# Kernel tuning notes

Measured on AMD Instinct MI355X. Metric: run time of the kernel, lower is better.

The kernel has to match this reference:

```python
import math
import jax, jax.numpy as jnp
import numpy as np

S = 2048
D_MOD = 1024
D_K = 64
D_V = 64
H = 16
MASKED = True


def setup_inputs() -> dict:
    key = jax.random.key(0)
    ks = jax.random.split(key, 11)
    sc_in = 1.0 / math.sqrt(D_MOD)
    sc_o = 1.0 / math.sqrt(H * D_V)
    return {
        "Q_input": jax.random.normal(ks[0], (S, D_MOD), jnp.float32),
        "K_input": jax.random.normal(ks[1], (S, D_MOD), jnp.float32),
        "V_input": jax.random.normal(ks[2], (S, D_MOD), jnp.float32),
        # stacked per-head Linear params (torch Linear: y = x @ W.T + b)
        "WQw": jax.random.uniform(ks[3], (H, D_K, D_MOD), jnp.float32, -sc_in, sc_in),
        "WQb": jax.random.uniform(ks[4], (H, D_K), jnp.float32, -sc_in, sc_in),
        "WKw": jax.random.uniform(ks[5], (H, D_K, D_MOD), jnp.float32, -sc_in, sc_in),
        "WKb": jax.random.uniform(ks[6], (H, D_K), jnp.float32, -sc_in, sc_in),
        "WVw": jax.random.uniform(ks[7], (H, D_V, D_MOD), jnp.float32, -sc_in, sc_in),
        "WVb": jax.random.uniform(ks[8], (H, D_V), jnp.float32, -sc_in, sc_in),
        "WOw": jax.random.uniform(ks[9], (D_MOD, H * D_V), jnp.float32, -sc_o, sc_o),
        "WOb": jax.random.uniform(ks[10], (D_MOD,), jnp.float32, -sc_o, sc_o),
    }


def reference(Q_input, K_input, V_input, WQw, WQb, WKw, WKb, WVw, WVb, WOw, WOb):
    # per-head projections, batched over heads: [H, S, d]
    q = jnp.einsum("sd,hkd->hsk", Q_input, WQw) + WQb[:, None, :]
    k = jnp.einsum("sd,hkd->hsk", K_input, WKw) + WKb[:, None, :]
    v = jnp.einsum("sd,hvd->hsv", V_input, WVw) + WVb[:, None, :]
    # raw scores [H, S, T]
    qk = jnp.einsum("hsk,htk->hst", q, k)
    if MASKED:
        qk = jnp.tril(qk)  # torch.tril: zero (not -inf) upper triangle
    # torch log_softmax(dim=0) on each [S, T] matrix -> axis 1 of [H, S, T]
    scores = jax.nn.log_softmax(qk / math.sqrt(D_K), axis=1)
    attn = jnp.einsum("hst,htv->hsv", scores, v)  # [H, S, d_v]
    # torch.cat(head_attns, dim=1) -> [S, H*d_v], head-major feature order
    Z = jnp.transpose(attn, (1, 0, 2)).reshape(S, H * D_V)
    return Z @ WOw.T + WOb
```

## Files before the change

kernel.cpp:

```cpp
#include <hip/hip_runtime.h>
#include <math.h>
#include <stdint.h>

#define S 2048
#define DMOD 1024
#define H 16

typedef unsigned short ushort_t;
typedef short bf16x8 __attribute__((ext_vector_type(8)));
typedef float f32x4 __attribute__((ext_vector_type(4)));

#define SW(r) ((((r) & 7)) ^ ((((r) >> 3) & 3) << 1))

__device__ __forceinline__ ushort_t f2b(float f) {
    union { float f; unsigned u; } x; x.f = f;
    return (ushort_t)((x.u + 0x7FFFu + ((x.u >> 16) & 1u)) >> 16);
}
__device__ __forceinline__ float b2f(ushort_t b) {
    union { unsigned u; float f; } x; x.u = ((unsigned)b) << 16;
    return x.f;
}
__device__ __forceinline__ void gld16(const ushort_t* g, ushort_t* l) {
    __builtin_amdgcn_global_load_lds(
        (const __attribute__((address_space(1))) unsigned int*)g,
        (__attribute__((address_space(3))) unsigned int*)l, 16, 0, 0);
}

__global__ __launch_bounds__(256) void init_all(
    float* __restrict__ attn_raw, float* __restrict__ out,
    float* __restrict__ sumexp, float* __restrict__ corr)
{
    const int b = blockIdx.x;
    const float4 z4 = {0.f, 0.f, 0.f, 0.f};
    if (b < 2048) {
        *(float4*)(attn_raw + ((size_t)b * 256 + threadIdx.x) * 4) = z4;
    } else if (b < 4096) {
        *(float4*)(out + ((size_t)(b - 2048) * 256 + threadIdx.x) * 4) = z4;
    } else if (b < 4128) {
        int e = ((b - 4096) * 256 + threadIdx.x) * 4;
        float4 v = {(float)(e & 2047), (float)((e + 1) & 2047),
                    (float)((e + 2) & 2047), (float)((e + 3) & 2047)};
        *(float4*)(sumexp + e) = v;
    } else {
        *(float4*)(corr + threadIdx.x * 4) = z4;
    }
}

__global__ __launch_bounds__(256) void convert_all(
    const float* q, const float* k, const float* v,
    const float* wq, const float* wk, const float* wv, const float* wo,
    ushort_t* qo, ushort_t* ko, ushort_t* vo,
    ushort_t* wqo, ushort_t* wko, ushort_t* wvo, ushort_t* woo)
{
    const int seg = blockIdx.y;
    const float* src; ushort_t* dst; size_t off = 0;
    const size_t M1 = (size_t)1 << 20;
    if (seg < 2)       { src = q;  dst = qo;  off = (size_t)seg * M1; }
    else if (seg < 4)  { src = k;  dst = ko;  off = (size_t)(seg - 2) * M1; }
    else if (seg < 6)  { src = v;  dst = vo;  off = (size_t)(seg - 4) * M1; }
    else if (seg == 6) { src = wq; dst = wqo; }
    else if (seg == 7) { src = wk; dst = wko; }
    else if (seg == 8) { src = wv; dst = wvo; }
    else               { src = wo; dst = woo; }
    size_t i = off + ((size_t)blockIdx.x * 256 + threadIdx.x) * 4;
    float4 f = *(const float4*)(src + i);
    union { uint2 u2; ushort_t us[4]; } o;
    o.us[0] = f2b(f.x); o.us[1] = f2b(f.y); o.us[2] = f2b(f.z); o.us[3] = f2b(f.w);
    *(uint2*)(dst + i) = o.u2;
}

__global__ __launch_bounds__(256) void gemm_qkv(
    const ushort_t* __restrict__ A0, const ushort_t* __restrict__ A1,
    const ushort_t* __restrict__ A2, const ushort_t* __restrict__ Wqkv,
    const float* __restrict__ b0, const float* __restrict__ b1,
    const float* __restrict__ b2,
    ushort_t* __restrict__ qbb, ushort_t* __restrict__ kbb,
    ushort_t* __restrict__ vt)
{
    __shared__ ushort_t As[128 * 64];
    __shared__ ushort_t Bs[64 * 64];
    const int tid = threadIdx.x;
    const int lane = tid & 63, wid = tid >> 6;
    const int quad = lane >> 4, l15 = lane & 15;
    const int wr = wid >> 1, wc = wid & 1;
    const int m0 = blockIdx.y * 128;
    const int n0 = blockIdx.x * 64;
    const int seg = n0 >> 10;
    const int nloc = n0 & 1023;
    const ushort_t* A = seg == 0 ? A0 : (seg == 1 ? A1 : A2);
    const float* bias = seg == 0 ? b0 : (seg == 1 ? b1 : b2);

    const f32x4 fz = {0.f, 0.f, 0.f, 0.f};
    f32x4 acc[4][2];
#pragma unroll
    for (int i = 0; i < 4; ++i) { acc[i][0] = fz; acc[i][1] = fz; }

    for (int k0 = 0; k0 < DMOD; k0 += 64) {
        __syncthreads();
#pragma unroll
        for (int i = 0; i < 4; ++i) {
            int c = i * 256 + tid, row = c >> 3, kcl = c & 7;
            gld16(A + (size_t)(m0 + row) * DMOD + k0 + (kcl ^ SW(row)) * 8, &As[c * 8]);
        }
#pragma unroll
        for (int i = 0; i < 2; ++i) {
            int c = i * 256 + tid, row = c >> 3, kcl = c & 7;
            gld16(Wqkv + (size_t)(n0 + row) * DMOD + k0 + (kcl ^ SW(row)) * 8, &Bs[c * 8]);
        }
        __syncthreads();
#pragma unroll
        for (int kc = 0; kc < 2; ++kc) {
            bf16x8 af[4], bfr[2];
#pragma unroll
            for (int mi = 0; mi < 4; ++mi) {
                int row = wr * 64 + mi * 16 + l15;
                af[mi] = *(const bf16x8*)&As[row * 64 + ((kc * 4 + quad) ^ SW(row)) * 8];
            }
#pragma unroll
            for (int ni = 0; ni < 2; ++ni) {
                int row = wc * 32 + ni * 16 + l15;
                bfr[ni] = *(const bf16x8*)&Bs[row * 64 + ((kc * 4 + quad) ^ SW(row)) * 8];
            }
#pragma unroll
            for (int mi = 0; mi < 4; ++mi)
#pragma unroll
                for (int ni = 0; ni < 2; ++ni)
                    acc[mi][ni] = __builtin_amdgcn_mfma_f32_16x16x32_bf16(
                        af[mi], bfr[ni], acc[mi][ni], 0, 0, 0);
        }
    }

    if (seg < 2) {
        ushort_t* C = seg == 0 ? qbb : kbb;
#pragma unroll
        for (int mi = 0; mi < 4; ++mi)
#pragma unroll
            for (int ni = 0; ni < 2; ++ni) {
                int gn = nloc + wc * 32 + ni * 16 + l15;
                float bv = bias[gn];
#pragma unroll
                for (int r = 0; r < 4; ++r) {
                    int gm = m0 + wr * 64 + mi * 16 + quad * 4 + r;
                    C[(size_t)gm * DMOD + gn] = f2b(acc[mi][ni][r] + bv);
                }
            }
    } else {
#pragma unroll
        for (int mi = 0; mi < 4; ++mi)
#pragma unroll
            for (int ni = 0; ni < 2; ++ni) {
                int gn = nloc + wc * 32 + ni * 16 + l15;
                float bv = bias[gn];
                int gmb = m0 + wr * 64 + mi * 16 + quad * 4;
                union { uint2 u2; ushort_t us[4]; } o;
#pragma unroll
                for (int r = 0; r < 4; ++r) o.us[r] = f2b(acc[mi][ni][r] + bv);
                *(uint2*)&vt[(size_t)gn * S + gmb] = o.u2;
            }
    }
}

__global__ __launch_bounds__(512, 4) void attn_mfma(
    const ushort_t* __restrict__ qb, const ushort_t* __restrict__ kb,
    const ushort_t* __restrict__ vt, float* __restrict__ attn_raw,
    float* __restrict__ sumexp)
{
    __shared__ ushort_t Qs[128 * 64];
    __shared__ ushort_t Ks[2][4096];
    __shared__ ushort_t Vs[2][4096];
    __shared__ ushort_t Ps[128 * 64];
    __shared__ float    sacc[1024];

    const int h = blockIdx.y;
    const int bx = blockIdx.x;
    const int si = 15 - (bx >> 1);
    const int z = bx & 1;
    const int half = si + 1;
    const int tbeg = z ? half : 0;
    const int tend = z ? 2 * si + 2 : half;
    const int s0 = si * 128;

    const int tid = threadIdx.x;
    const int lane = tid & 63, w = tid >> 6;
    const int quad = lane >> 4, l15 = lane & 15;
    const int sband = s0 + w * 16;

    const ushort_t* qh = qb + h * 64;
    const ushort_t* kh = kb + h * 64;
    const ushort_t* vh = vt + (size_t)(h * 64) * S;

#pragma unroll
    for (int i = 0; i < 2; ++i) {
        int c = i * 512 + tid, row = c >> 3, kcl = c & 7;
        gld16(qh + (size_t)(s0 + row) * DMOD + (kcl ^ SW(row)) * 8, &Qs[c * 8]);
    }
    {
        int t0 = tbeg * 64;
        int row = tid >> 3, kcl = tid & 7;
        gld16(kh + (size_t)(t0 + row) * DMOD + (kcl ^ SW(row)) * 8, &Ks[0][tid * 8]);
        gld16(vh + (size_t)row * S + t0 + (kcl ^ SW(row)) * 8, &Vs[0][tid * 8]);
    }
    for (int i = tid; i < 1024; i += 512) sacc[i] = 0.f;
    __syncthreads();

    bf16x8 aq[2];
    {
        int rq = w * 16 + l15;
#pragma unroll
        for (int kc = 0; kc < 2; ++kc)
            aq[kc] = *(const bf16x8*)&Qs[rq * 64 + ((kc * 4 + quad) ^ SW(rq)) * 8];
    }

    const f32x4 fz = {0.f, 0.f, 0.f, 0.f};
    f32x4 oacc[4];
#pragma unroll
    for (int ni = 0; ni < 4; ++ni) oacc[ni] = fz;

    for (int it = tbeg; it < tend; ++it) {
        const int p = (it - tbeg) & 1;
        const int t0 = it * 64;
        if (it + 1 < tend) {
            int t1 = t0 + 64;
            int row = tid >> 3, kcl = tid & 7;
            gld16(kh + (size_t)(t1 + row) * DMOD + (kcl ^ SW(row)) * 8, &Ks[1 - p][tid * 8]);
            gld16(vh + (size_t)row * S + t1 + (kcl ^ SW(row)) * 8, &Vs[1 - p][tid * 8]);
        }

        if (t0 < sband + 16) {
            f32x4 xf[4];
#pragma unroll
            for (int ti = 0; ti < 4; ++ti) xf[ti] = fz;
#pragma unroll
            for (int kc = 0; kc < 2; ++kc) {
#pragma unroll
                for (int ti = 0; ti < 4; ++ti) {
                    int rk = ti * 16 + l15;
                    bf16x8 bk = *(const bf16x8*)&Ks[p][rk * 64 + ((kc * 4 + quad) ^ SW(rk)) * 8];
                    xf[ti] = __builtin_amdgcn_mfma_f32_16x16x32_bf16(aq[kc], bk, xf[ti], 0, 0, 0);
                }
            }

            const bool clean = (t0 + 63 <= sband);
            const int s_q = sband + quad * 4;
#pragma unroll
            for (int ti = 0; ti < 4; ++ti) {
                int t_g = t0 + ti * 16 + l15;
                float es = 0.f;
#pragma unroll
                for (int r = 0; r < 4; ++r) {
                    float xv = xf[ti][r] * 0.125f;
                    bool live = clean || (s_q + r >= t_g);
                    xv = live ? xv : 0.f;
                    es += live ? __expf(xv) : 0.f;
                    xf[ti][r] = xv;
                }
                es += __shfl_xor(es, 16, 64);
                es += __shfl_xor(es, 32, 64);
                if (quad == 0) atomicAdd(&sacc[t0 - tbeg * 64 + ti * 16 + l15], es);
#pragma unroll
                for (int r = 0; r < 4; ++r) {
                    int sl = w * 16 + quad * 4 + r;
                    int tc = ti * 16 + l15;
                    Ps[sl * 64 + ((tc >> 3) ^ SW(sl)) * 8 + (tc & 7)] = f2b(xf[ti][r]);
                }
            }

#pragma unroll
            for (int kc = 0; kc < 2; ++kc) {
                int rp = w * 16 + l15;
                bf16x8 ap = *(const bf16x8*)&Ps[rp * 64 + ((kc * 4 + quad) ^ SW(rp)) * 8];
#pragma unroll
                for (int ni = 0; ni < 4; ++ni) {
                    int rv = ni * 16 + l15;
                    bf16x8 bv = *(const bf16x8*)&Vs[p][rv * 64 + ((kc * 4 + quad) ^ SW(rv)) * 8];
                    oacc[ni] = __builtin_amdgcn_mfma_f32_16x16x32_bf16(ap, bv, oacc[ni], 0, 0, 0);
                }
            }
        }
        __syncthreads();
    }

    {
        int nv = (tend - tbeg) * 64;
        for (int i = tid; i < nv; i += 512)
            atomicAdd(&sumexp[h * S + tbeg * 64 + i], sacc[i]);
    }
#pragma unroll
    for (int ni = 0; ni < 4; ++ni)
#pragma unroll
        for (int r = 0; r < 4; ++r) {
            int s_g = s0 + w * 16 + quad * 4 + r;
            atomicAdd(&attn_raw[(size_t)s_g * DMOD + h * 64 + ni * 16 + l15],
                      oacc[ni][r]);
        }
}

__global__ __launch_bounds__(256) void corr_kernel(
    const float* __restrict__ sumexp, const ushort_t* __restrict__ vt,
    float* __restrict__ corr)
{
    const int w = threadIdx.x >> 6, lane = threadIdx.x & 63;
    const int r = blockIdx.x * 4 + w;
    const int h = r >> 6;
    float acc = 0.f;
#pragma unroll
    for (int i = 0; i < 4; ++i) {
        int t = i * 512 + lane * 8;
        bf16x8 vv = *(const bf16x8*)&vt[(size_t)r * S + t];
        float4 s0 = *(const float4*)&sumexp[h * S + t];
        float4 s1 = *(const float4*)&sumexp[h * S + t + 4];
        acc += logf(s0.x) * b2f((ushort_t)vv[0]) + logf(s0.y) * b2f((ushort_t)vv[1])
             + logf(s0.z) * b2f((ushort_t)vv[2]) + logf(s0.w) * b2f((ushort_t)vv[3])
             + logf(s1.x) * b2f((ushort_t)vv[4]) + logf(s1.y) * b2f((ushort_t)vv[5])
             + logf(s1.z) * b2f((ushort_t)vv[6]) + logf(s1.w) * b2f((ushort_t)vv[7]);
    }
#pragma unroll
    for (int d = 1; d < 64; d <<= 1) acc += __shfl_xor(acc, d, 64);
    if (lane == 0) corr[r] = acc;
}

__global__ __launch_bounds__(256) void convert_Z(
    const float* __restrict__ attn_raw, const float* __restrict__ corr,
    ushort_t* __restrict__ Zb)
{
    size_t i = ((size_t)blockIdx.x * 256 + threadIdx.x) * 4;
    float4 f = *(const float4*)(attn_raw + i);
    int c = (int)(i & (DMOD - 1));
    union { uint2 u2; ushort_t us[4]; } o;
    o.us[0] = f2b(f.x - corr[c]);
    o.us[1] = f2b(f.y - corr[c + 1]);
    o.us[2] = f2b(f.z - corr[c + 2]);
    o.us[3] = f2b(f.w - corr[c + 3]);
    *(uint2*)(Zb + i) = o.u2;
}

__global__ __launch_bounds__(256) void gemm_out(
    const ushort_t* __restrict__ A, const ushort_t* __restrict__ W,
    const float* __restrict__ bias, float* __restrict__ C)
{
    __shared__ ushort_t As[128 * 64];
    __shared__ ushort_t Bs[64 * 64];
    const int tid = threadIdx.x;
    const int lane = tid & 63, wid = tid >> 6;
    const int quad = lane >> 4, l15 = lane & 15;
    const int wr = wid >> 1, wc = wid & 1;
    const int m0 = blockIdx.y * 128, n0 = blockIdx.x * 64;
    const int kbeg = blockIdx.z * 512, kend = kbeg + 512;

    const f32x4 fz = {0.f, 0.f, 0.f, 0.f};
    f32x4 acc[4][2];
#pragma unroll
    for (int i = 0; i < 4; ++i) { acc[i][0] = fz; acc[i][1] = fz; }

    for (int k0 = kbeg; k0 < kend; k0 += 64) {
        __syncthreads();
#pragma unroll
        for (int i = 0; i < 4; ++i) {
            int c = i * 256 + tid, row = c >> 3, kcl = c & 7;
            gld16(A + (size_t)(m0 + row) * DMOD + k0 + (kcl ^ SW(row)) * 8, &As[c * 8]);
        }
#pragma unroll
        for (int i = 0; i < 2; ++i) {
            int c = i * 256 + tid, row = c >> 3, kcl = c & 7;
            gld16(W + (size_t)(n0 + row) * DMOD + k0 + (kcl ^ SW(row)) * 8, &Bs[c * 8]);
        }
        __syncthreads();
#pragma unroll
        for (int kc = 0; kc < 2; ++kc) {
            bf16x8 af[4], bfr[2];
#pragma unroll
            for (int mi = 0; mi < 4; ++mi) {
                int row = wr * 64 + mi * 16 + l15;
                af[mi] = *(const bf16x8*)&As[row * 64 + ((kc * 4 + quad) ^ SW(row)) * 8];
            }
#pragma unroll
            for (int ni = 0; ni < 2; ++ni) {
                int row = wc * 32 + ni * 16 + l15;
                bfr[ni] = *(const bf16x8*)&Bs[row * 64 + ((kc * 4 + quad) ^ SW(row)) * 8];
            }
#pragma unroll
            for (int mi = 0; mi < 4; ++mi)
#pragma unroll
                for (int ni = 0; ni < 2; ++ni)
                    acc[mi][ni] = __builtin_amdgcn_mfma_f32_16x16x32_bf16(
                        af[mi], bfr[ni], acc[mi][ni], 0, 0, 0);
        }
    }
#pragma unroll
    for (int mi = 0; mi < 4; ++mi)
#pragma unroll
        for (int ni = 0; ni < 2; ++ni) {
            int gn = n0 + wc * 32 + ni * 16 + l15;
            float bv = (kbeg == 0) ? bias[gn] : 0.f;
#pragma unroll
            for (int r = 0; r < 4; ++r) {
                int gm = m0 + wr * 64 + mi * 16 + quad * 4 + r;
                atomicAdd(&C[(size_t)gm * DMOD + gn], acc[mi][ni][r] + bv);
            }
        }
}

extern "C" void kernel_launch(void* const* d_in, const int* in_sizes, int n_in,
                              void* d_out, int out_size, void* d_ws, size_t ws_size,
                              hipStream_t stream) {
    const float* Qin = (const float*)d_in[0];
    const float* Kin = (const float*)d_in[1];
    const float* Vin = (const float*)d_in[2];
    const float* WQw = (const float*)d_in[3];
    const float* WQb = (const float*)d_in[4];
    const float* WKw = (const float*)d_in[5];
    const float* WKb = (const float*)d_in[6];
    const float* WVw = (const float*)d_in[7];
    const float* WVb = (const float*)d_in[8];
    const float* WOw = (const float*)d_in[9];
    const float* WOb = (const float*)d_in[10];

    float* ws = (float*)d_ws;
    const size_t M1 = (size_t)1 << 20;
    ushort_t* qbb  = (ushort_t*)(ws);
    ushort_t* kbb  = (ushort_t*)(ws + M1);
    ushort_t* vt   = (ushort_t*)(ws + 2 * M1);
    ushort_t* wqkv = (ushort_t*)(ws + 3 * M1);
    ushort_t* wob  = (ushort_t*)(ws + 4 * M1 + M1 / 2);
    ushort_t* Qbin = (ushort_t*)(ws + 5 * M1);
    ushort_t* Kbin = (ushort_t*)(ws + 6 * M1);
    ushort_t* Vbin = (ushort_t*)(ws + 7 * M1);
    float* attn_raw = ws + 6 * M1;
    ushort_t* Zb    = (ushort_t*)(ws + 5 * M1);
    float* sumexp   = ws + 8 * M1;
    float* corr     = ws + 8 * M1 + H * S;

    init_all<<<4129, 256, 0, stream>>>(attn_raw, (float*)d_out, sumexp, corr);

    convert_all<<<dim3(1024, 10), 256, 0, stream>>>(
        Qin, Kin, Vin, WQw, WKw, WVw, WOw,
        Qbin, Kbin, Vbin,
        wqkv, wqkv + (size_t)1024 * 1024, wqkv + (size_t)2 * 1024 * 1024, wob);

    gemm_qkv<<<dim3(48, 16), 256, 0, stream>>>(
        Qbin, Kbin, Vbin, wqkv, WQb, WKb, WVb, qbb, kbb, vt);

    attn_mfma<<<dim3(32, H), 512, 0, stream>>>(qbb, kbb, vt, attn_raw, sumexp);

    corr_kernel<<<256, 256, 0, stream>>>(sumexp, vt, corr);
    convert_Z<<<2048, 256, 0, stream>>>(attn_raw, corr, Zb);

    gemm_out<<<dim3(16, 16, 2), 256, 0, stream>>>(Zb, wob, WOb, (float*)d_out);
}
```

Baseline: 203.8 us.

## Alias Q and P shared buffers, skip dead atomics, alternate block order per head

Merges the Q and P shared-memory tiles into one buffer, since Q is moved into registers before P is written. This cuts LDS use and may let more blocks fit per CU. It also reverses the causal-tile block order for half the heads to balance the schedule. Other changes: a branch separates clean tiles from masked tiles, a cheaper round-to-nearest bf16 conversion (no ties-to-even) replaces the old one, and the global atomic adds are skipped for waves that saw no live tiles. The cheaper rounding can change low bits slightly, and aliasing Q with P relies on the register load completing before the first P write.

```diff
diff --git a/kernel.cpp b/kernel.cpp
--- a/kernel.cpp
+++ b/kernel.cpp
@@ -15,6 +15,10 @@
 __device__ __forceinline__ ushort_t f2b(float f) {
     union { float f; unsigned u; } x; x.f = f;
     return (ushort_t)((x.u + 0x7FFFu + ((x.u >> 16) & 1u)) >> 16);
+}
+__device__ __forceinline__ ushort_t f2b_fast(float f) {
+    union { float f; unsigned u; } x; x.f = f;
+    return (ushort_t)((x.u + 0x8000u) >> 16);
 }
 __device__ __forceinline__ float b2f(ushort_t b) {
     union { unsigned u; float f; } x; x.u = ((unsigned)b) << 16;
@@ -165,15 +169,14 @@
     const ushort_t* __restrict__ vt, float* __restrict__ attn_raw,
     float* __restrict__ sumexp)
 {
-    __shared__ ushort_t Qs[128 * 64];
+    __shared__ ushort_t QPs[128 * 64];
     __shared__ ushort_t Ks[2][4096];
     __shared__ ushort_t Vs[2][4096];
-    __shared__ ushort_t Ps[128 * 64];
     __shared__ float    sacc[1024];
 
     const int h = blockIdx.y;
     const int bx = blockIdx.x;
-    const int si = 15 - (bx >> 1);
+    const int si = (h < 8) ? (15 - (bx >> 1)) : (bx >> 1);
     const int z = bx & 1;
     const int half = si + 1;
     const int tbeg = z ? half : 0;
@@ -192,7 +195,7 @@
 #pragma unroll
     for (int i = 0; i < 2; ++i) {
         int c = i * 512 + tid, row = c >> 3, kcl = c & 7;
-        gld16(qh + (size_t)(s0 + row) * DMOD + (kcl ^ SW(row)) * 8, &Qs[c * 8]);
+        gld16(qh + (size_t)(s0 + row) * DMOD + (kcl ^ SW(row)) * 8, &QPs[c * 8]);
     }
     {
         int t0 = tbeg * 64;
@@ -208,13 +211,14 @@
         int rq = w * 16 + l15;
 #pragma unroll
         for (int kc = 0; kc < 2; ++kc)
-            aq[kc] = *(const bf16x8*)&Qs[rq * 64 + ((kc * 4 + quad) ^ SW(rq)) * 8];
+            aq[kc] = *(const bf16x8*)&QPs[rq * 64 + ((kc * 4 + quad) ^ SW(rq)) * 8];
     }
 
     const f32x4 fz = {0.f, 0.f, 0.f, 0.f};
     f32x4 oacc[4];
 #pragma unroll
     for (int ni = 0; ni < 4; ++ni) oacc[ni] = fz;
+    bool any_live = false;
 
     for (int it = tbeg; it < tend; ++it) {
         const int p = (it - tbeg) & 1;
@@ -227,6 +231,7 @@
         }
 
         if (t0 < sband + 16) {
+            any_live = true;
             f32x4 xf[4];
 #pragma unroll
             for (int ti = 0; ti < 4; ++ti) xf[ti] = fz;
@@ -246,29 +251,38 @@
             for (int ti = 0; ti < 4; ++ti) {
                 int t_g = t0 + ti * 16 + l15;
                 float es = 0.f;
-#pragma unroll
-                for (int r = 0; r < 4; ++r) {
-                    float xv = xf[ti][r] * 0.125f;
-                    bool live = clean || (s_q + r >= t_g);
-                    xv = live ? xv : 0.f;
-                    es += live ? __expf(xv) : 0.f;
-                    xf[ti][r] = xv;
+                if (clean) {
+#pragma unroll
+                    for (int r = 0; r < 4; ++r) {
+                        float xv = xf[ti][r] * 0.125f;
+                        es += __expf(xv);
+                        xf[ti][r] = xv;
+                    }
+                } else {
+#pragma unroll
+                    for (int r = 0; r < 4; ++r) {
+                        float xv = xf[ti][r] * 0.125f;
+                        bool live = (s_q + r >= t_g);
+                        xv = live ? xv : 0.f;
+                        es += live ? __expf(xv) : 0.f;
+                        xf[ti][r] = xv;
+                    }
                 }
                 es += __shfl_xor(es, 16, 64);
                 es += __shfl_xor(es, 32, 64);
-                if (quad == 0) atomicAdd(&sacc[t0 - tbeg * 64 + ti * 16 + l15], es);
+                if (quad == 0) atomicAdd(&sacc[(it - tbeg) * 64 + ti * 16 + l15], es);
 #pragma unroll
                 for (int r = 0; r < 4; ++r) {
                     int sl = w * 16 + quad * 4 + r;
                     int tc = ti * 16 + l15;
-                    Ps[sl * 64 + ((tc >> 3) ^ SW(sl)) * 8 + (tc & 7)] = f2b(xf[ti][r]);
+                    QPs[sl * 64 + ((tc >> 3) ^ SW(sl)) * 8 + (tc & 7)] = f2b_fast(xf[ti][r]);
                 }
             }
 
 #pragma unroll
             for (int kc = 0; kc < 2; ++kc) {
                 int rp = w * 16 + l15;
-                bf16x8 ap = *(const bf16x8*)&Ps[rp * 64 + ((kc * 4 + quad) ^ SW(rp)) * 8];
+                bf16x8 ap = *(const bf16x8*)&QPs[rp * 64 + ((kc * 4 + quad) ^ SW(rp)) * 8];
 #pragma unroll
                 for (int ni = 0; ni < 4; ++ni) {
                     int rv = ni * 16 + l15;
@@ -285,14 +299,16 @@
         for (int i = tid; i < nv; i += 512)
             atomicAdd(&sumexp[h * S + tbeg * 64 + i], sacc[i]);
     }
-#pragma unroll
-    for (int ni = 0; ni < 4; ++ni)
-#pragma unroll
-        for (int r = 0; r < 4; ++r) {
-            int s_g = s0 + w * 16 + quad * 4 + r;
-            atomicAdd(&attn_raw[(size_t)s_g * DMOD + h * 64 + ni * 16 + l15],
-                      oacc[ni][r]);
-        }
+    if (any_live) {
+#pragma unroll
+        for (int ni = 0; ni < 4; ++ni)
+#pragma unroll
+            for (int r = 0; r < 4; ++r) {
+                int s_g = s0 + w * 16 + quad * 4 + r;
+                atomicAdd(&attn_raw[(size_t)s_g * DMOD + h * 64 + ni * 16 + l15],
+                          oacc[ni][r]);
+            }
+    }
 }
 
 __global__ __launch_bounds__(256) void corr_kernel(
```

New measurement: 189.1 us. -7.2%, faster.
